# Kernel optimization log

Measured on AMD Instinct MI355X. Metric: run time of the kernel, lower is better.

The kernel has to match this reference:

```python
import jax, jax.numpy as jnp
import numpy as np
from jax import lax

KERNEL_SIZE = 3
SMOOTH_NR = 0.0
SMOOTH_DR = 1e-5


def _box_sum(x, k):
    # 3D box-filter sum with zero padding (matches F.conv3d padding=(k-1)//2),
    # x: [B, C, H, W, D]. 'SAME' padding with odd k and stride 1 == symmetric pad (k-1)//2.
    return lax.reduce_window(x, jnp.array(0.0, x.dtype), lax.add,
                             window_dimensions=(1, 1, k, k, k),
                             window_strides=(1, 1, 1, 1, 1),
                             padding='SAME')


def setup_inputs() -> dict:
    key = jax.random.key(0)
    k1, k2 = jax.random.split(key)
    shape = (2, 1, 192, 192, 192)
    pred = jax.random.uniform(k1, shape, dtype=jnp.float32)
    target = jax.random.uniform(k2, shape, dtype=jnp.float32)
    return {"pred": pred, "target": target}


def reference(pred, target):
    k = KERNEL_SIZE
    kvol = float(k ** 3)
    # Local means of I, J, I^2, J^2, I*J (box filter divided by kernel volume,
    # mirroring the torch code's avg_filt grouped conv over the 5C-channel interm).
    mI = _box_sum(pred, k) / kvol
    mJ = _box_sum(target, k) / kvol
    mII = _box_sum(pred * pred, k) / kvol
    mJJ = _box_sum(target * target, k) / kvol
    mIJ = _box_sum(pred * target, k) / kvol
    # Fused NCC reduction (cc3d_fwd_interm_v1): convert means back to
    # windowed sums-based cross/variance terms using kernel_vol.
    cross = kvol * (mIJ - mI * mJ)
    p_var = kvol * (mII - mI * mI)
    t_var = kvol * (mJJ - mJ * mJ)
    ncc = (cross * cross + SMOOTH_NR) / (t_var * p_var + SMOOTH_DR)
    # reduction='mean', loss is negated squared local ZNCC
    return -jnp.mean(ncc)
```

## Files before the change

### kernel.cpp

```cpp
#include <hip/hip_runtime.h>

#define DIMB 2
#define DIMS 192
#define DPT 4
#define TX 16
#define TY 16
#define HCHUNK 6
#define ROWF 72
#define PLANE_F 1296
#define BUF_F 2816
#define NSEG 11

#define GLOAD_LDS16(gp, lp) __builtin_amdgcn_global_load_lds( \
    (const __attribute__((address_space(1))) void*)(gp),      \
    (__attribute__((address_space(3))) void*)(lp), 16, 0, 0)

__device__ __forceinline__ float dpp_left(float x) {
    const int i = __float_as_int(x);
    return __int_as_float(__builtin_amdgcn_update_dpp(i, i, 0x111, 0xf, 0xf, false));
}
__device__ __forceinline__ float dpp_right(float x) {
    const int i = __float_as_int(x);
    return __int_as_float(__builtin_amdgcn_update_dpp(i, i, 0x101, 0xf, 0xf, false));
}

__device__ __forceinline__ float ncc_row3(const float (&Pm)[5][DPT],
                                          const float (&Pc)[5][DPT],
                                          const float (&Pn)[5][DPT])
{
    const float inv = 1.0f / 27.0f;
    float acc = 0.f;
#pragma unroll
    for (int j = 0; j < DPT; ++j) {
        const float sI  = Pm[0][j] + Pc[0][j] + Pn[0][j];
        const float sJ  = Pm[1][j] + Pc[1][j] + Pn[1][j];
        const float sII = Pm[2][j] + Pc[2][j] + Pn[2][j];
        const float sJJ = Pm[3][j] + Pc[3][j] + Pn[3][j];
        const float sIJ = Pm[4][j] + Pc[4][j] + Pn[4][j];
        const float uI = sI * inv;
        const float uJ = sJ * inv;
        const float cross = sIJ - uI * sJ;
        const float pvar  = sII - uI * sI;
        const float tvar  = sJJ - uJ * sJ;
        acc += (cross * cross) * __builtin_amdgcn_rcpf(tvar * pvar + 1e-5f);
    }
    return acc;
}

__global__ __launch_bounds__(256)
void FusedLocalNormalizedCrossCorrelationLoss_37838661877790_kernel(
    const float* __restrict__ pred, const float* __restrict__ targ,
    double* __restrict__ acc_out)
{
    __shared__ float L[2][BUF_F];

    const int tx = threadIdx.x, ty = threadIdx.y;
    const int tid = ty * TX + tx;
    const int lane = tid & 63, wv = tid >> 6;
    const int d0b = blockIdx.x * (TX * DPT);
    const int w0  = blockIdx.y * TY;
    const int bz  = blockIdx.z;
    const int b   = bz >> 5;
    const int h0  = (bz & 31) * HCHUNK;

    int   sl[3]; int co[3]; const float* ab[3];
#pragma unroll
    for (int i = 0; i < 3; ++i) {
        const int s = wv + 4 * i;
        const int ss = (s < NSEG) ? s : 0;
        const int fi = ss * 256 + lane * 4;
        const int a  = (fi >= PLANE_F) ? 1 : 0;
        int fi2 = fi - a * PLANE_F;
        if (fi2 > PLANE_F - 1) fi2 = PLANE_F - 1;
        const int r = fi2 / ROWF, c = fi2 % ROWF;
        int gd = d0b - 4 + c;
        gd = gd < 0 ? 0 : (gd > DIMS - 4 ? DIMS - 4 : gd);
        int wr = w0 - 1 + r;
        wr = wr < 0 ? 0 : (wr > DIMS - 1 ? DIMS - 1 : wr);
        sl[i] = ss * 256;
        co[i] = wr * DIMS + gd;
        ab[i] = a ? targ : pred;
    }

    auto stage = [&](int buf, int hh) {
        const int hhc = hh < 0 ? 0 : (hh > DIMS - 1 ? DIMS - 1 : hh);
        const size_t po = ((size_t)b * DIMS + hhc) * (DIMS * DIMS);
#pragma unroll
        for (int i = 0; i < 3; ++i) {
            if (wv + 4 * i >= NSEG) break;
            GLOAD_LDS16(ab[i] + po + co[i], &L[buf][sl[i]]);
        }
    };

    const bool lo_mask = (tx == 0)      && (blockIdx.x == 0);
    const bool hi_mask = (tx == TX - 1) && (blockIdx.x == gridDim.x - 1);
    const int rb0 = 4 * tx;

    auto plane = [&](int buf, int hh, float (&P)[5][DPT]) {
#pragma unroll
        for (int c5 = 0; c5 < 5; ++c5)
#pragma unroll
            for (int j = 0; j < DPT; ++j) P[c5][j] = 0.f;
        if (hh < 0 || hh >= DIMS) return;
        const float* Lp = &L[buf][0];
        const float* Lt = &L[buf][PLANE_F];
#pragma unroll
        for (int dw = 0; dw < 3; ++dw) {
            const int wr = w0 + ty + dw - 1;
            if (wr < 0 || wr >= DIMS) continue;
            const int rb = (ty + dw) * ROWF + rb0;
            const float4 pm = *reinterpret_cast<const float4*>(Lp + rb + 4);
            const float4 tm = *reinterpret_cast<const float4*>(Lt + rb + 4);
            float p0 = dpp_left (pm.w);
            float p5 = dpp_right(pm.x);
            float t0 = dpp_left (tm.w);
            float t5 = dpp_right(tm.x);
            if (tx == 0)      { p0 = Lp[rb + 3]; t0 = Lt[rb + 3]; }
            if (tx == TX - 1) { p5 = Lp[rb + 8]; t5 = Lt[rb + 8]; }
            if (lo_mask) { p0 = 0.f; t0 = 0.f; }
            if (hi_mask) { p5 = 0.f; t5 = 0.f; }
            const float pv[6] = {p0, pm.x, pm.y, pm.z, pm.w, p5};
            const float tv[6] = {t0, tm.x, tm.y, tm.z, tm.w, t5};
            float pp[6], tt[6], pt[6];
#pragma unroll
            for (int k = 0; k < 6; ++k) {
                pp[k] = pv[k] * pv[k];
                tt[k] = tv[k] * tv[k];
                pt[k] = pv[k] * tv[k];
            }
#define WSUM(dst, a)                                            \
            { const float c12 = a[1] + a[2], c34 = a[3] + a[4]; \
              dst[0] += a[0] + c12; dst[1] += c12 + a[3];       \
              dst[2] += a[2] + c34; dst[3] += c34 + a[5]; }
            WSUM(P[0], pv)
            WSUM(P[1], tv)
            WSUM(P[2], pp)
            WSUM(P[3], tt)
            WSUM(P[4], pt)
#undef WSUM
        }
    };

    float PA[5][DPT], PB[5][DPT], PC[5][DPT];
    float acc = 0.f;

    stage(0, h0 - 1);
    stage(1, h0);
    __syncthreads();
    plane(0, h0 - 1, PA);
    __syncthreads();
    stage(0, h0 + 1);
    plane(1, h0, PB);
    __syncthreads();
    stage(1, h0 + 2);
    plane(0, h0 + 1, PC);  acc += ncc_row3(PA, PB, PC);
    __syncthreads();
    stage(0, h0 + 3);
    plane(1, h0 + 2, PA);  acc += ncc_row3(PB, PC, PA);
    __syncthreads();
    stage(1, h0 + 4);
    plane(0, h0 + 3, PB);  acc += ncc_row3(PC, PA, PB);
    __syncthreads();
    stage(0, h0 + 5);
    plane(1, h0 + 4, PC);  acc += ncc_row3(PA, PB, PC);
    __syncthreads();
    stage(1, h0 + 6);
    plane(0, h0 + 5, PA);  acc += ncc_row3(PB, PC, PA);
    __syncthreads();
    plane(1, h0 + 6, PB);  acc += ncc_row3(PC, PA, PB);

#pragma unroll
    for (int off = 32; off > 0; off >>= 1)
        acc += __shfl_down(acc, off, 64);
    __shared__ float wacc[4];
    if ((tid & 63) == 0) wacc[tid >> 6] = acc;
    __syncthreads();
    if (tid == 0) {
        const double s = (double)wacc[0] + (double)wacc[1]
                       + (double)wacc[2] + (double)wacc[3];
        atomicAdd(acc_out, s);
    }
}

__global__ void ncc_finalize(const double* __restrict__ acc,
                             float* __restrict__ out)
{
    const double n = (double)((size_t)DIMB * DIMS * DIMS * DIMS);
    out[0] = (float)(-acc[0] / n);
}

extern "C" void kernel_launch(void* const* d_in, const int* in_sizes, int n_in,
                              void* d_out, int out_size, void* d_ws, size_t ws_size,
                              hipStream_t stream) {
    const float* pred = (const float*)d_in[0];
    const float* targ = (const float*)d_in[1];
    double* acc = (double*)d_ws;

    hipMemsetAsync(d_ws, 0, sizeof(double), stream);

    dim3 block(TX, TY, 1);
    dim3 grid(DIMS / (TX * DPT), DIMS / TY, DIMB * (DIMS / HCHUNK));
    FusedLocalNormalizedCrossCorrelationLoss_37838661877790_kernel
        <<<grid, block, 0, stream>>>(pred, targ, acc);
    ncc_finalize<<<1, 1, 0, stream>>>(acc, (float*)d_out);
}
```

Baseline: 172.7 us.

## Give each wave a private LDS slab and replace block barriers with vmcnt waits

```diff
diff --git a/kernel.cpp b/kernel.cpp
--- a/kernel.cpp
+++ b/kernel.cpp
@@ -7,13 +7,15 @@
 #define TY 16
 #define HCHUNK 6
 #define ROWF 72
-#define PLANE_F 1296
-#define BUF_F 2816
-#define NSEG 11
+#define ARR_F 432
+#define SLAB_F 1024
 
 #define GLOAD_LDS16(gp, lp) __builtin_amdgcn_global_load_lds( \
     (const __attribute__((address_space(1))) void*)(gp),      \
     (__attribute__((address_space(3))) void*)(lp), 16, 0, 0)
+
+#define WAITV(n) asm volatile("s_waitcnt vmcnt(" #n ")" ::: "memory")
+#define LGKM0    asm volatile("s_waitcnt lgkmcnt(0)" ::: "memory")
 
 __device__ __forceinline__ float dpp_left(float x) {
     const int i = __float_as_int(x);
@@ -52,63 +54,60 @@
     const float* __restrict__ pred, const float* __restrict__ targ,
     double* __restrict__ acc_out)
 {
-    __shared__ float L[2][BUF_F];
+    __shared__ float L[4][2][SLAB_F];
 
     const int tx = threadIdx.x, ty = threadIdx.y;
     const int tid = ty * TX + tx;
     const int lane = tid & 63, wv = tid >> 6;
+    const int tyw = ty & 3;
     const int d0b = blockIdx.x * (TX * DPT);
     const int w0  = blockIdx.y * TY;
     const int bz  = blockIdx.z;
     const int b   = bz >> 5;
     const int h0  = (bz & 31) * HCHUNK;
 
-    int   sl[3]; int co[3]; const float* ab[3];
+    int co[4]; const float* ab[4];
 #pragma unroll
-    for (int i = 0; i < 3; ++i) {
-        const int s = wv + 4 * i;
-        const int ss = (s < NSEG) ? s : 0;
-        const int fi = ss * 256 + lane * 4;
-        const int a  = (fi >= PLANE_F) ? 1 : 0;
-        int fi2 = fi - a * PLANE_F;
-        if (fi2 > PLANE_F - 1) fi2 = PLANE_F - 1;
-        const int r = fi2 / ROWF, c = fi2 % ROWF;
-        int gd = d0b - 4 + c;
+    for (int c = 0; c < 4; ++c) {
+        const int fi = c * 256 + lane * 4;
+        const int a  = (fi >= ARR_F) ? 1 : 0;
+        int fi2 = fi - a * ARR_F;
+        if (fi2 > ARR_F - 4) fi2 = ARR_F - 4;
+        const int r = fi2 / ROWF, cl = fi2 % ROWF;
+        int gd = d0b - 4 + cl;
         gd = gd < 0 ? 0 : (gd > DIMS - 4 ? DIMS - 4 : gd);
-        int wr = w0 - 1 + r;
+        int wr = w0 - 1 + 4 * wv + r;
         wr = wr < 0 ? 0 : (wr > DIMS - 1 ? DIMS - 1 : wr);
-        sl[i] = ss * 256;
-        co[i] = wr * DIMS + gd;
-        ab[i] = a ? targ : pred;
+        co[c] = wr * DIMS + gd;
+        ab[c] = a ? targ : pred;
     }
 
-    auto stage = [&](int buf, int hh) {
+    auto stage = [&](int slot, int hh) {
         const int hhc = hh < 0 ? 0 : (hh > DIMS - 1 ? DIMS - 1 : hh);
         const size_t po = ((size_t)b * DIMS + hhc) * (DIMS * DIMS);
+        float* lb = &L[wv][slot][0];
 #pragma unroll
-        for (int i = 0; i < 3; ++i) {
-            if (wv + 4 * i >= NSEG) break;
-            GLOAD_LDS16(ab[i] + po + co[i], &L[buf][sl[i]]);
-        }
+        for (int c = 0; c < 4; ++c)
+            GLOAD_LDS16(ab[c] + po + co[c], lb + c * 256);
     };
 
     const bool lo_mask = (tx == 0)      && (blockIdx.x == 0);
     const bool hi_mask = (tx == TX - 1) && (blockIdx.x == gridDim.x - 1);
     const int rb0 = 4 * tx;
 
-    auto plane = [&](int buf, int hh, float (&P)[5][DPT]) {
+    auto plane = [&](int slot, int hh, float (&P)[5][DPT]) {
 #pragma unroll
         for (int c5 = 0; c5 < 5; ++c5)
 #pragma unroll
             for (int j = 0; j < DPT; ++j) P[c5][j] = 0.f;
         if (hh < 0 || hh >= DIMS) return;
-        const float* Lp = &L[buf][0];
-        const float* Lt = &L[buf][PLANE_F];
+        const float* Lp = &L[wv][slot][0];
+        const float* Lt = Lp + ARR_F;
 #pragma unroll
         for (int dw = 0; dw < 3; ++dw) {
             const int wr = w0 + ty + dw - 1;
             if (wr < 0 || wr >= DIMS) continue;
-            const int rb = (ty + dw) * ROWF + rb0;
+            const int rb = (tyw + dw) * ROWF + rb0;
             const float4 pm = *reinterpret_cast<const float4*>(Lp + rb + 4);
             const float4 tm = *reinterpret_cast<const float4*>(Lt + rb + 4);
             float p0 = dpp_left (pm.w);
@@ -146,28 +145,20 @@
 
     stage(0, h0 - 1);
     stage(1, h0);
-    __syncthreads();
-    plane(0, h0 - 1, PA);
-    __syncthreads();
-    stage(0, h0 + 1);
-    plane(1, h0, PB);
-    __syncthreads();
-    stage(1, h0 + 2);
-    plane(0, h0 + 1, PC);  acc += ncc_row3(PA, PB, PC);
-    __syncthreads();
-    stage(0, h0 + 3);
-    plane(1, h0 + 2, PA);  acc += ncc_row3(PB, PC, PA);
-    __syncthreads();
-    stage(1, h0 + 4);
-    plane(0, h0 + 3, PB);  acc += ncc_row3(PC, PA, PB);
-    __syncthreads();
-    stage(0, h0 + 5);
-    plane(1, h0 + 4, PC);  acc += ncc_row3(PA, PB, PC);
-    __syncthreads();
-    stage(1, h0 + 6);
-    plane(0, h0 + 5, PA);  acc += ncc_row3(PB, PC, PA);
-    __syncthreads();
-    plane(1, h0 + 6, PB);  acc += ncc_row3(PC, PA, PB);
+    WAITV(4); plane(0, h0 - 1, PA); LGKM0; stage(0, h0 + 1);
+    WAITV(4); plane(1, h0,     PB); LGKM0; stage(1, h0 + 2);
+    WAITV(4); plane(0, h0 + 1, PC); LGKM0; stage(0, h0 + 3);
+    acc += ncc_row3(PA, PB, PC);
+    WAITV(4); plane(1, h0 + 2, PA); LGKM0; stage(1, h0 + 4);
+    acc += ncc_row3(PB, PC, PA);
+    WAITV(4); plane(0, h0 + 3, PB); LGKM0; stage(0, h0 + 5);
+    acc += ncc_row3(PC, PA, PB);
+    WAITV(4); plane(1, h0 + 4, PC); LGKM0; stage(1, h0 + 6);
+    acc += ncc_row3(PA, PB, PC);
+    WAITV(4); plane(0, h0 + 5, PA);
+    acc += ncc_row3(PB, PC, PA);
+    WAITV(0); plane(1, h0 + 6, PB);
+    acc += ncc_row3(PC, PA, PB);
 
 #pragma unroll
     for (int off = 32; off > 0; off >>= 1)
```

After: 155.5 us. -10.0%, faster.
